# Kernel optimization log

Measured on AMD Instinct MI355X. Metric: run time of the kernel, lower is better.

The kernel has to match this reference:

```python
import jax, jax.numpy as jnp
import numpy as np

D_MODEL = 1024
D_STATE = 16
D_CONV = 4
EXPAND = 2
D_INNER = D_MODEL * EXPAND
BATCH = 4
SEQLEN = 4096


def setup_inputs() -> dict:
    key = jax.random.key(0)
    ks = jax.random.split(key, 10)
    s = 1.0 / np.sqrt(D_MODEL)
    si = 1.0 / np.sqrt(D_INNER)
    return {
        "x": jax.random.normal(ks[0], (BATCH, SEQLEN, D_MODEL), jnp.float32),
        "x_proj_w": jax.random.normal(ks[1], (D_INNER, D_MODEL), jnp.float32) * s,
        "dt_proj_w": jax.random.normal(ks[2], (D_INNER, D_MODEL), jnp.float32) * s,
        "dt_proj_b": jax.random.normal(ks[3], (D_INNER,), jnp.float32) * 0.1,
        "A_log": jax.random.normal(ks[4], (D_INNER, D_STATE), jnp.float32),
        "D": jnp.ones((D_INNER,), jnp.float32),
        "B_proj_w": jax.random.normal(ks[5], (D_STATE, D_MODEL), jnp.float32) * s,
        "C_proj_w": jax.random.normal(ks[6], (D_STATE, D_MODEL), jnp.float32) * s,
        "conv_w": jax.random.normal(ks[7], (D_INNER, 1, D_CONV), jnp.float32) * 0.5,
        "conv_b": jax.random.normal(ks[8], (D_INNER,), jnp.float32) * 0.1,
        "out_proj_w": jax.random.normal(ks[9], (D_MODEL, D_INNER), jnp.float32) * si,
    }


def _selective_scan(xc, delta, A, B, C, D):
    # xc, delta: (b, L, d_inner); B, C: (b, L, d_state); A: (d_inner, d_state)
    batch, seqlen, d_inner = xc.shape
    d_state = A.shape[1]

    def step(h, inp):
        x_t, dt, B_t, C_t = inp  # (b,di), (b,di), (b,ds), (b,ds)
        A_disc = jnp.exp(dt[:, :, None] * A[None])           # (b, di, ds)
        h = A_disc * h + (dt[:, :, None] * B_t[:, None, :]) * x_t[:, :, None]
        y_t = jnp.einsum('bds,bs->bd', h, C_t) + D[None, :] * x_t
        return h, y_t

    h0 = jnp.zeros((batch, d_inner, d_state), xc.dtype)
    xs = (jnp.swapaxes(xc, 0, 1), jnp.swapaxes(delta, 0, 1),
          jnp.swapaxes(B, 0, 1), jnp.swapaxes(C, 0, 1))
    _, ys = jax.lax.scan(step, h0, xs)  # ys: (L, b, d_inner)
    return jnp.swapaxes(ys, 0, 1)


def reference(x, x_proj_w, dt_proj_w, dt_proj_b, A_log, D, B_proj_w, C_proj_w, conv_w, conv_b, out_proj_w):
    seqlen = x.shape[1]
    x_inner = x @ x_proj_w.T  # (b, L, d_inner)
    # causal depthwise conv1d: torch pads both sides by d_conv-1 then keeps first L,
    # equivalent to left-pad (d_conv-1, 0)
    xc = jax.lax.conv_general_dilated(
        jnp.swapaxes(x_inner, 1, 2), conv_w,
        window_strides=(1,), padding=[(D_CONV - 1, 0)],
        dimension_numbers=('NCH', 'OIH', 'NCH'),
        feature_group_count=D_INNER)
    xc = jnp.swapaxes(xc + conv_b[None, :, None], 1, 2)
    xc = jax.nn.silu(xc)
    B = x @ B_proj_w.T
    C = x @ C_proj_w.T
    delta = jax.nn.softplus(x @ dt_proj_w.T + dt_proj_b)
    A = -jnp.exp(A_log.astype(jnp.float32))
    y = _selective_scan(xc, delta, A, B, C, D)
    return y @ out_proj_w.T
```

## Files before the change

kernel.cpp:

```cpp
#include <hip/hip_runtime.h>
#include <hip/hip_bf16.h>
#include <math.h>

typedef __bf16 bf16;
typedef __bf16 bf16x2 __attribute__((ext_vector_type(2)));
typedef __bf16 bf16x8 __attribute__((ext_vector_type(8)));
typedef float f32x4 __attribute__((ext_vector_type(4)));

#define AS_G __attribute__((address_space(1)))
#define AS_L __attribute__((address_space(3)))

__device__ __forceinline__ void async_ld16(const void* g, void* l) {
  __builtin_amdgcn_global_load_lds((const AS_G void*)g, (AS_L void*)l, 16, 0, 0);
}
__device__ __forceinline__ float fexp2(float x) { return __builtin_amdgcn_exp2f(x); }

__global__ void detect_dtype(const void* __restrict__ Dones, int* __restrict__ flag) {
  if (threadIdx.x == 0 && blockIdx.x == 0) {
    *flag = (*(const unsigned int*)Dones == 0x3F803F80u) ? 0 : 1;
  }
}

__global__ __launch_bounds__(256) void to_bf16(
    const void* __restrict__ src, bf16* __restrict__ dst, int n8,
    const int* __restrict__ flag)
{
  const int i = blockIdx.x * 256 + threadIdx.x;
  if (i >= n8) return;
  bf16x8 o;
  if (*flag) {
    const f32x4* s = (const f32x4*)src;
    f32x4 a = s[2*i], b = s[2*i + 1];
    #pragma unroll
    for (int e = 0; e < 4; ++e) { o[e] = (bf16)a[e]; o[e+4] = (bf16)b[e]; }
  } else {
    o = ((const bf16x8*)src)[i];
  }
  ((bf16x8*)dst)[i] = o;
}

template<int EPI>
__global__ __launch_bounds__(256, 2) void gemm_bt(
    const bf16* __restrict__ A, const bf16* __restrict__ W,
    bf16* __restrict__ OutB, float* __restrict__ OutF,
    const bf16* __restrict__ bias, const int* __restrict__ flag,
    int M, int N, int K)
{
  __shared__ bf16 smA[128*32];
  __shared__ bf16 smB[128*32];
  const int tid  = threadIdx.x;
  const int wave = tid >> 6;
  const int lane = tid & 63;
  const int m0 = blockIdx.x * 128;
  const int n0 = blockIdx.y * 128;
  const int wm = (wave >> 1) * 64;
  const int wn = (wave & 1) * 64;
  const int lm = lane & 15;
  const int q  = lane >> 4;
  const bool f32o = (EPI == 2) && (*flag != 0);

  f32x4 acc[4][4] = {};

  const int chunk0 = wave*128 + lane;
  const int chunk1 = wave*128 + 64 + lane;
  const int r0 = chunk0 >> 2, c0 = chunk0 & 3;
  const int r1 = chunk1 >> 2, c1 = chunk1 & 3;
  const bf16* gA0 = A + (size_t)(m0 + r0)*K + c0*8;
  const bf16* gA1 = A + (size_t)(m0 + r1)*K + c1*8;
  const bf16* gB0 = W + (size_t)(n0 + r0)*K + c0*8;
  const bf16* gB1 = W + (size_t)(n0 + r1)*K + c1*8;
  bf16* lA0 = smA + (size_t)(wave*128     )*8;
  bf16* lA1 = smA + (size_t)(wave*128 + 64)*8;
  bf16* lB0 = smB + (size_t)(wave*128     )*8;
  bf16* lB1 = smB + (size_t)(wave*128 + 64)*8;

  for (int k0 = 0; k0 < K; k0 += 32) {
    __syncthreads();
    async_ld16(gA0 + k0, lA0);
    async_ld16(gA1 + k0, lA1);
    async_ld16(gB0 + k0, lB0);
    async_ld16(gB1 + k0, lB1);
    __syncthreads();
    bf16x8 af[4], bfr[4];
    #pragma unroll
    for (int mi = 0; mi < 4; ++mi)
      af[mi] = *(const bf16x8*)(smA + (wm + mi*16 + lm)*32 + q*8);
    #pragma unroll
    for (int ni = 0; ni < 4; ++ni)
      bfr[ni] = *(const bf16x8*)(smB + (wn + ni*16 + lm)*32 + q*8);
    #pragma unroll
    for (int mi = 0; mi < 4; ++mi)
      #pragma unroll
      for (int ni = 0; ni < 4; ++ni)
        acc[mi][ni] = __builtin_amdgcn_mfma_f32_16x16x32_bf16(af[mi], bfr[ni], acc[mi][ni], 0, 0, 0);
  }

  #pragma unroll
  for (int mi = 0; mi < 4; ++mi) {
    #pragma unroll
    for (int ni = 0; ni < 4; ++ni) {
      const int col = n0 + wn + ni*16 + lm;
      float bval = 0.f;
      if (EPI == 1) bval = (float)bias[col];
      #pragma unroll
      for (int r = 0; r < 4; ++r) {
        const int row = m0 + wm + mi*16 + q*4 + r;
        float v = acc[mi][ni][r];
        if (EPI == 1) {
          v += bval;
          v = (v > 20.f) ? v : log1pf(__expf(v));
        }
        const size_t idx = (size_t)row*N + col;
        if (EPI == 2 && f32o) OutF[idx] = v;
        else                  OutB[idx] = (bf16)v;
      }
    }
  }
}

__global__ __launch_bounds__(64) void bc_gemm(
    const bf16* __restrict__ X,
    const bf16* __restrict__ Bw, const bf16* __restrict__ Cw,
    float* __restrict__ Bout, float* __restrict__ Cout)
{
  const int lane = threadIdx.x;
  const int lm = lane & 15, q = lane >> 4;
  const int m0 = blockIdx.x * 16;
  const bf16* W = blockIdx.y ? Cw : Bw;
  float* O      = blockIdx.y ? Cout : Bout;
  f32x4 acc = {};
  const bf16* pa = X + (size_t)(m0 + lm)*1024 + q*8;
  const bf16* pw = W + (size_t)lm*1024 + q*8;
  for (int k0 = 0; k0 < 1024; k0 += 32) {
    bf16x8 a = *(const bf16x8*)(pa + k0);
    bf16x8 w = *(const bf16x8*)(pw + k0);
    acc = __builtin_amdgcn_mfma_f32_16x16x32_bf16(a, w, acc, 0, 0, 0);
  }
  #pragma unroll
  for (int r = 0; r < 4; ++r)
    O[(size_t)(m0 + q*4 + r)*16 + lm] = acc[r];
}

__global__ __launch_bounds__(256) void conv_silu(
    const bf16* __restrict__ Xin, const bf16* __restrict__ cw,
    const bf16* __restrict__ cb, bf16* __restrict__ Xc)
{
  const int idx = blockIdx.x * 256 + threadIdx.x;
  const int row = idx >> 8;
  const int dv  = (idx & 255) * 8;
  const int t   = row & 4095;
  bf16x8 wv[4];
  const bf16x8* pw = (const bf16x8*)(cw + (size_t)dv*4);
  #pragma unroll
  for (int j = 0; j < 4; ++j) wv[j] = pw[j];
  bf16x8 bv = *(const bf16x8*)(cb + dv);
  float acc[8];
  #pragma unroll
  for (int e = 0; e < 8; ++e) acc[e] = (float)bv[e];
  #pragma unroll
  for (int j = 0; j < 4; ++j) {
    const int tr = t - 3 + j;
    if (tr < 0) continue;
    bf16x8 xv = *(const bf16x8*)(Xin + (size_t)(row - 3 + j)*2048 + dv);
    #pragma unroll
    for (int e = 0; e < 8; ++e) {
      const int li = e*4 + j;
      acc[e] += (float)xv[e] * (float)wv[li >> 3][li & 7];
    }
  }
  bf16x8 o;
  #pragma unroll
  for (int e = 0; e < 8; ++e) {
    float v = acc[e];
    v = v / (1.f + __expf(-v));
    o[e] = (bf16)v;
  }
  *(bf16x8*)(Xc + (size_t)row*2048 + dv) = o;
}

__global__ __launch_bounds__(256) void scan_phase1(
    const bf16* __restrict__ Xc, const bf16* __restrict__ Dt,
    const float* __restrict__ Bm, const bf16* __restrict__ A_log,
    float* __restrict__ Hend, float* __restrict__ Dtsum)
{
  const int tid = threadIdx.x;
  const int d0 = blockIdx.x * 512 + tid * 2;
  const int c = blockIdx.y;
  const int b = blockIdx.z;
  const int t0 = c * 128;
  __shared__ float sB[128*16];
  {
    const f32x4* src = (const f32x4*)(Bm + ((size_t)b*4096 + t0)*16);
    f32x4* dst = (f32x4*)sB;
    dst[tid]       = src[tid];
    dst[tid + 256] = src[tid + 256];
  }
  __syncthreads();
  float A2[2][16];
  #pragma unroll
  for (int u = 0; u < 2; ++u)
    #pragma unroll
    for (int s = 0; s < 16; ++s)
      A2[u][s] = -__expf((float)A_log[(d0+u)*16 + s]) * 1.44269504088896f;
  float h[2][16] = {};
  float dts[2] = {0.f, 0.f};
  const bf16* pX = Xc + ((size_t)b*4096 + t0)*2048 + d0;
  const bf16* pD = Dt + ((size_t)b*4096 + t0)*2048 + d0;
  bf16x2 vD = *(const bf16x2*)pD;
  bf16x2 vX = *(const bf16x2*)pX;
  for (int t = 0; t < 128; ++t) {
    bf16x2 nD = vD, nX = vX;
    if (t < 127) {
      nD = *(const bf16x2*)(pD + (size_t)(t+1)*2048);
      nX = *(const bf16x2*)(pX + (size_t)(t+1)*2048);
    }
    f32x4 Bv[4];
    #pragma unroll
    for (int i = 0; i < 4; ++i) Bv[i] = ((const f32x4*)(sB + t*16))[i];
    #pragma unroll
    for (int u = 0; u < 2; ++u) {
      const float dt = (float)vD[u];
      const float xv = (float)vX[u];
      dts[u] += dt;
      const float dx = dt * xv;
      #pragma unroll
      for (int s = 0; s < 16; ++s) {
        const float ad = fexp2(dt * A2[u][s]);
        h[u][s] = ad*h[u][s] + dx * Bv[s>>2][s&3];
      }
    }
    vD = nD; vX = nX;
  }
  #pragma unroll
  for (int u = 0; u < 2; ++u) {
    const size_t base = (((size_t)b*32 + c)*2048 + d0 + u)*16;
    #pragma unroll
    for (int s = 0; s < 16; ++s) Hend[base + s] = h[u][s];
    Dtsum[((size_t)b*32 + c)*2048 + d0 + u] = dts[u];
  }
}

__global__ __launch_bounds__(256) void scan_phase2(
    float* __restrict__ H,
    const float* __restrict__ Dtsum,
    const bf16* __restrict__ A_log)
{
  const int idx = blockIdx.x*256 + threadIdx.x;
  const int s = idx & 15;
  const int d = (idx >> 4) & 2047;
  const int b = idx >> 15;
  const float A2 = -__expf((float)A_log[d*16 + s]) * 1.44269504088896f;
  float h = 0.f;
  for (int c = 0; c < 32; ++c) {
    const size_t off = (((size_t)b*32 + c)*2048 + d)*16 + s;
    const float hend = H[off];
    H[off] = h;
    const float ap = fexp2(A2 * Dtsum[((size_t)b*32 + c)*2048 + d]);
    h = h*ap + hend;
  }
}

__global__ __launch_bounds__(256) void scan_phase3(
    const bf16* __restrict__ Xc, const bf16* __restrict__ Dt,
    const float* __restrict__ Bm, const float* __restrict__ Cm,
    const bf16* __restrict__ A_log, const bf16* __restrict__ Dvec,
    const float* __restrict__ Hstart, bf16* __restrict__ Y)
{
  const int tid = threadIdx.x;
  const int d0 = blockIdx.x * 512 + tid * 2;
  const int c = blockIdx.y;
  const int b = blockIdx.z;
  const int t0 = c * 128;
  __shared__ float sB[128*16];
  __shared__ float sC[128*16];
  {
    const f32x4* srcB = (const f32x4*)(Bm + ((size_t)b*4096 + t0)*16);
    const f32x4* srcC = (const f32x4*)(Cm + ((size_t)b*4096 + t0)*16);
    ((f32x4*)sB)[tid]       = srcB[tid];
    ((f32x4*)sB)[tid + 256] = srcB[tid + 256];
    ((f32x4*)sC)[tid]       = srcC[tid];
    ((f32x4*)sC)[tid + 256] = srcC[tid + 256];
  }
  __syncthreads();
  float A2[2][16];
  #pragma unroll
  for (int u = 0; u < 2; ++u)
    #pragma unroll
    for (int s = 0; s < 16; ++s)
      A2[u][s] = -__expf((float)A_log[(d0+u)*16 + s]) * 1.44269504088896f;
  float h[2][16];
  #pragma unroll
  for (int u = 0; u < 2; ++u) {
    const size_t base = (((size_t)b*32 + c)*2048 + d0 + u)*16;
    #pragma unroll
    for (int s = 0; s < 16; ++s) h[u][s] = Hstart[base + s];
  }
  const float Dd0 = (float)Dvec[d0];
  const float Dd1 = (float)Dvec[d0 + 1];
  const bf16* pX = Xc + ((size_t)b*4096 + t0)*2048 + d0;
  const bf16* pD = Dt + ((size_t)b*4096 + t0)*2048 + d0;
  bf16*       pY = Y  + ((size_t)b*4096 + t0)*2048 + d0;
  bf16x2 vD = *(const bf16x2*)pD;
  bf16x2 vX = *(const bf16x2*)pX;
  for (int t = 0; t < 128; ++t) {
    bf16x2 nD = vD, nX = vX;
    if (t < 127) {
      nD = *(const bf16x2*)(pD + (size_t)(t+1)*2048);
      nX = *(const bf16x2*)(pX + (size_t)(t+1)*2048);
    }
    f32x4 Bv[4], Cv[4];
    #pragma unroll
    for (int i = 0; i < 4; ++i) {
      Bv[i] = ((const f32x4*)(sB + t*16))[i];
      Cv[i] = ((const f32x4*)(sC + t*16))[i];
    }
    float y[2];
    #pragma unroll
    for (int u = 0; u < 2; ++u) {
      const float dt = (float)vD[u];
      const float xv = (float)vX[u];
      const float dx = dt * xv;
      y[u] = (u ? Dd1 : Dd0) * xv;
      #pragma unroll
      for (int s = 0; s < 16; ++s) {
        const float ad = fexp2(dt * A2[u][s]);
        h[u][s] = ad*h[u][s] + dx * Bv[s>>2][s&3];
        y[u] += h[u][s] * Cv[s>>2][s&3];
      }
    }
    bf16x2 yo; yo[0] = (bf16)y[0]; yo[1] = (bf16)y[1];
    *(bf16x2*)(pY + (size_t)t*2048) = yo;
    vD = nD; vX = nX;
  }
}

extern "C" void kernel_launch(void* const* d_in, const int* in_sizes, int n_in,
                              void* d_out, int out_size, void* d_ws, size_t ws_size,
                              hipStream_t stream)
{
  char* ws = (char*)d_ws;
  size_t off = 0;
  auto alloc = [&](size_t bytes) -> char* {
    char* p = ws + off; off += (bytes + 255) & ~(size_t)255; return p;
  };
  bf16*  xin = (bf16*) alloc((size_t)16384*2048*2);
  bf16*  dlt = (bf16*) alloc((size_t)16384*2048*2);
  bf16*  xc  = (bf16*) alloc((size_t)16384*2048*2);
  float* Bm  = (float*)alloc((size_t)16384*16*4);
  float* Cm  = (float*)alloc((size_t)16384*16*4);
  float* Hst = (float*)alloc((size_t)4*32*2048*16*4);
  float* Dts = (float*)alloc((size_t)4*32*2048*4);
  int*   flag = (int*) alloc(256);
  const int ncanon = 11;
  static const int canon_n[11] = {
    4*4096*1024, 2048*1024, 2048*1024, 2048, 2048*16, 2048,
    16*1024, 16*1024, 2048*4, 2048, 1024*2048 };
  bf16* canon[11];
  for (int i = 0; i < ncanon; ++i) canon[i] = (bf16*)alloc((size_t)canon_n[i]*2);
  if (off > ws_size) return;

  detect_dtype<<<1, 64, 0, stream>>>(d_in[5], flag);
  for (int i = 0; i < ncanon; ++i) {
    const int n8 = canon_n[i] / 8;
    to_bf16<<<(n8 + 255)/256, 256, 0, stream>>>(d_in[i], canon[i], n8, flag);
  }
  const bf16* x          = canon[0];
  const bf16* x_proj_w   = canon[1];
  const bf16* dt_proj_w  = canon[2];
  const bf16* dt_proj_b  = canon[3];
  const bf16* A_log      = canon[4];
  const bf16* Dvec       = canon[5];
  const bf16* B_proj_w   = canon[6];
  const bf16* C_proj_w   = canon[7];
  const bf16* conv_w     = canon[8];
  const bf16* conv_b     = canon[9];
  const bf16* out_proj_w = canon[10];

  gemm_bt<0><<<dim3(128,16), 256, 0, stream>>>(x, x_proj_w,  xin, nullptr, nullptr,   flag, 16384, 2048, 1024);
  gemm_bt<1><<<dim3(128,16), 256, 0, stream>>>(x, dt_proj_w, dlt, nullptr, dt_proj_b, flag, 16384, 2048, 1024);
  bc_gemm<<<dim3(1024,2), 64, 0, stream>>>(x, B_proj_w, C_proj_w, Bm, Cm);
  conv_silu<<<dim3(16384), 256, 0, stream>>>(xin, conv_w, conv_b, xc);
  scan_phase1<<<dim3(4,32,4), 256, 0, stream>>>(xc, dlt, Bm, A_log, Hst, Dts);
  scan_phase2<<<dim3(512),    256, 0, stream>>>(Hst, Dts, A_log);
  scan_phase3<<<dim3(4,32,4), 256, 0, stream>>>(xc, dlt, Bm, Cm, A_log, Dvec, Hst, xin );
  gemm_bt<2><<<dim3(128,8), 256, 0, stream>>>(xin, out_proj_w, (bf16*)d_out, (float*)d_out, nullptr, flag, 16384, 1024, 2048);
}
```

Baseline: 725.3 us.

## Double-buffer GEMM LDS tiles, swizzle LDS layout, and swap block grid order

The bf16 GEMM now keeps two LDS buffers so the async global-to-LDS load of the next K tile is issued while the current tile is multiplied. The 16-byte chunk index within each LDS row is XOR-swizzled by row to reduce bank conflicts on the fragment reads. The grid is also transposed so consecutive blocks share an A row-block across different N tiles, which should improve L2 reuse of the activations. It doubles LDS per block, which may affect occupancy at two blocks per CU, and the loop assumes K is a multiple of 64.

```diff
diff --git a/kernel.cpp b/kernel.cpp
--- a/kernel.cpp
+++ b/kernel.cpp
@@ -46,13 +46,13 @@
     const bf16* __restrict__ bias, const int* __restrict__ flag,
     int M, int N, int K)
 {
-  __shared__ bf16 smA[128*32];
-  __shared__ bf16 smB[128*32];
+  __shared__ bf16 smA[2][128*32];
+  __shared__ bf16 smB[2][128*32];
   const int tid  = threadIdx.x;
   const int wave = tid >> 6;
   const int lane = tid & 63;
-  const int m0 = blockIdx.x * 128;
-  const int n0 = blockIdx.y * 128;
+  const int n0 = blockIdx.x * 128;
+  const int m0 = blockIdx.y * 128;
   const int wm = (wave >> 1) * 64;
   const int wn = (wave & 1) * 64;
   const int lm = lane & 15;
@@ -61,38 +61,55 @@
 
   f32x4 acc[4][4] = {};
 
-  const int chunk0 = wave*128 + lane;
-  const int chunk1 = wave*128 + 64 + lane;
-  const int r0 = chunk0 >> 2, c0 = chunk0 & 3;
-  const int r1 = chunk1 >> 2, c1 = chunk1 & 3;
+  const int ch0 = wave*128 + lane;
+  const int ch1 = ch0 + 64;
+  const int r0 = ch0 >> 2, c0 = (ch0 & 3) ^ ((r0 >> 1) & 3);
+  const int r1 = ch1 >> 2, c1 = (ch1 & 3) ^ ((r1 >> 1) & 3);
   const bf16* gA0 = A + (size_t)(m0 + r0)*K + c0*8;
   const bf16* gA1 = A + (size_t)(m0 + r1)*K + c1*8;
   const bf16* gB0 = W + (size_t)(n0 + r0)*K + c0*8;
   const bf16* gB1 = W + (size_t)(n0 + r1)*K + c1*8;
-  bf16* lA0 = smA + (size_t)(wave*128     )*8;
-  bf16* lA1 = smA + (size_t)(wave*128 + 64)*8;
-  bf16* lB0 = smB + (size_t)(wave*128     )*8;
-  bf16* lB1 = smB + (size_t)(wave*128 + 64)*8;
-
-  for (int k0 = 0; k0 < K; k0 += 32) {
-    __syncthreads();
-    async_ld16(gA0 + k0, lA0);
-    async_ld16(gA1 + k0, lA1);
-    async_ld16(gB0 + k0, lB0);
-    async_ld16(gB1 + k0, lB1);
-    __syncthreads();
+
+  int ofsA[4], ofsB[4];
+  #pragma unroll
+  for (int mi = 0; mi < 4; ++mi) {
+    const int row = wm + mi*16 + lm;
+    ofsA[mi] = row*32 + (q ^ ((row >> 1) & 3))*8;
+  }
+  #pragma unroll
+  for (int ni = 0; ni < 4; ++ni) {
+    const int row = wn + ni*16 + lm;
+    ofsB[ni] = row*32 + (q ^ ((row >> 1) & 3))*8;
+  }
+
+  auto stage = [&](int bfi, int k) {
+    async_ld16(gA0 + k, &smA[bfi][wave*1024      ]);
+    async_ld16(gA1 + k, &smA[bfi][wave*1024 + 512]);
+    async_ld16(gB0 + k, &smB[bfi][wave*1024      ]);
+    async_ld16(gB1 + k, &smB[bfi][wave*1024 + 512]);
+  };
+  auto compute = [&](int bfi) {
     bf16x8 af[4], bfr[4];
     #pragma unroll
-    for (int mi = 0; mi < 4; ++mi)
-      af[mi] = *(const bf16x8*)(smA + (wm + mi*16 + lm)*32 + q*8);
-    #pragma unroll
-    for (int ni = 0; ni < 4; ++ni)
-      bfr[ni] = *(const bf16x8*)(smB + (wn + ni*16 + lm)*32 + q*8);
+    for (int mi = 0; mi < 4; ++mi) af[mi]  = *(const bf16x8*)(&smA[bfi][ofsA[mi]]);
+    #pragma unroll
+    for (int ni = 0; ni < 4; ++ni) bfr[ni] = *(const bf16x8*)(&smB[bfi][ofsB[ni]]);
     #pragma unroll
     for (int mi = 0; mi < 4; ++mi)
       #pragma unroll
       for (int ni = 0; ni < 4; ++ni)
         acc[mi][ni] = __builtin_amdgcn_mfma_f32_16x16x32_bf16(af[mi], bfr[ni], acc[mi][ni], 0, 0, 0);
+  };
+
+  const int nIter = K >> 5;
+  stage(0, 0);
+  for (int i = 0; i < nIter; i += 2) {
+    __syncthreads();
+    stage(1, (i + 1) << 5);
+    compute(0);
+    __syncthreads();
+    if (i + 2 < nIter) stage(0, (i + 2) << 5);
+    compute(1);
   }
 
   #pragma unroll
@@ -376,12 +393,12 @@
   const bf16* conv_b     = canon[9];
   const bf16* out_proj_w = canon[10];
 
-  gemm_bt<0><<<dim3(128,16), 256, 0, stream>>>(x, x_proj_w,  xin, nullptr, nullptr,   flag, 16384, 2048, 1024);
-  gemm_bt<1><<<dim3(128,16), 256, 0, stream>>>(x, dt_proj_w, dlt, nullptr, dt_proj_b, flag, 16384, 2048, 1024);
+  gemm_bt<0><<<dim3(16,128), 256, 0, stream>>>(x, x_proj_w,  xin, nullptr, nullptr,   flag, 16384, 2048, 1024);
+  gemm_bt<1><<<dim3(16,128), 256, 0, stream>>>(x, dt_proj_w, dlt, nullptr, dt_proj_b, flag, 16384, 2048, 1024);
   bc_gemm<<<dim3(1024,2), 64, 0, stream>>>(x, B_proj_w, C_proj_w, Bm, Cm);
   conv_silu<<<dim3(16384), 256, 0, stream>>>(xin, conv_w, conv_b, xc);
   scan_phase1<<<dim3(4,32,4), 256, 0, stream>>>(xc, dlt, Bm, A_log, Hst, Dts);
   scan_phase2<<<dim3(512),    256, 0, stream>>>(Hst, Dts, A_log);
   scan_phase3<<<dim3(4,32,4), 256, 0, stream>>>(xc, dlt, Bm, Cm, A_log, Dvec, Hst, xin );
-  gemm_bt<2><<<dim3(128,8), 256, 0, stream>>>(xin, out_proj_w, (bf16*)d_out, (float*)d_out, nullptr, flag, 16384, 1024, 2048);
-}
+  gemm_bt<2><<<dim3(8,128), 256, 0, stream>>>(xin, out_proj_w, (bf16*)d_out, (float*)d_out, nullptr, flag, 16384, 1024, 2048);
+}
```

New measurement: 745.0 us. 2.7% more time.
